# Kernel optimization log

Measured on AMD Instinct MI355X. Metric: run time of the kernel, lower is better.

## Reference

```python
import jax, jax.numpy as jnp
import numpy as np

D_MODEL = 2048
HEAD_DIM = 128

def setup_inputs() -> dict:
    key = jax.random.key(0)
    ks = jax.random.split(key, 7)
    s = 1.0 / np.sqrt(D_MODEL)
    x = jax.random.normal(ks[0], (4, 4096, D_MODEL), dtype=jnp.float32)
    Wq = jax.random.uniform(ks[1], (D_MODEL, HEAD_DIM), jnp.float32, -s, s)
    bq = jax.random.uniform(ks[2], (HEAD_DIM,), jnp.float32, -s, s)
    Wk = jax.random.uniform(ks[3], (D_MODEL, HEAD_DIM), jnp.float32, -s, s)
    bk = jax.random.uniform(ks[4], (HEAD_DIM,), jnp.float32, -s, s)
    Wv = jax.random.uniform(ks[5], (D_MODEL, HEAD_DIM), jnp.float32, -s, s)
    bv = jax.random.uniform(ks[6], (HEAD_DIM,), jnp.float32, -s, s)
    return {"x": x, "Wq": Wq, "bq": bq, "Wk": Wk, "bk": bk, "Wv": Wv, "bv": bv}

def reference(x, Wq, bq, Wk, bk, Wv, bv):
    # x: [B, T, d_model]
    B, T, _ = x.shape
    q = jnp.einsum('btd,dh->bth', x, Wq) + bq  # [B,T,H]
    k = jnp.einsum('btd,dh->bth', x, Wk) + bk
    v = jnp.einsum('btd,dh->bth', x, Wv) + bv
    scores = jnp.einsum('bth,bsh->bts', q, k) / jnp.sqrt(jnp.float32(HEAD_DIM))  # [B,T,T]
    causal = jnp.tril(jnp.ones((T, T), dtype=bool))
    scores = jnp.where(causal[None], scores, -jnp.inf)
    probs = jax.nn.softmax(scores, axis=-1)
    return jnp.einsum('bts,bsh->bth', probs, v)  # [B,T,H]
```

## Files before the change

kernel.cpp:

```cpp
#include <hip/hip_runtime.h>
#include <math.h>

#define D_MODEL 2048
#define HD      128
#define NB      4
#define TT      4096
#define M_TOT   (NB * TT)
#define NCH     160
#define CHT     16

typedef __attribute__((ext_vector_type(8))) short bf16x8;
typedef __attribute__((ext_vector_type(4))) float f32x4;

__device__ __forceinline__ ushort f2bf(float f) {
    union { float f; unsigned int u; } v; v.f = f;
    unsigned int u = v.u;
    unsigned int r = (u + 0x7FFFu + ((u >> 16) & 1u)) >> 16;
    return (ushort)r;
}

__device__ __forceinline__ void gload_lds16(const void* g, void* l) {
    __builtin_amdgcn_global_load_lds(
        (const __attribute__((address_space(1))) unsigned int*)g,
        (__attribute__((address_space(3))) unsigned int*)l, 16, 0, 0);
}

__global__ __launch_bounds__(256) void wt_kernel(
        const float* __restrict__ Wq, const float* __restrict__ Wk,
        const float* __restrict__ Wv, ushort* __restrict__ WT) {
    const int p  = blockIdx.y;
    const int k0 = blockIdx.x * 128;
    const float* W = (p == 0) ? Wq : ((p == 1) ? Wk : Wv);

    __shared__ ushort Ts[128 * 136];

    const int tid = threadIdx.x;
    for (int i = 0; i < 64; i++) {
        int c  = i * 256 + tid;
        int kk = c >> 7, n = c & 127;
        Ts[n * 136 + kk] = f2bf(W[(size_t)(k0 + kk) * 128 + n]);
    }
    __syncthreads();
    for (int i = 0; i < 8; i++) {
        int c = i * 256 + tid;
        int n = c >> 4, j = c & 15;
        *(uint4*)(WT + (size_t)p * (128 * 2048) + (size_t)n * 2048 + k0 + j * 8) =
            *(const uint4*)&Ts[n * 136 + j * 8];
    }
}

__global__ __launch_bounds__(256, 3) void proj_fused(
        const float* __restrict__ x, const ushort* __restrict__ WT,
        const float* __restrict__ bq, const float* __restrict__ bk, const float* __restrict__ bv,
        ushort* __restrict__ Qb, ushort* __restrict__ Kb, ushort* __restrict__ Vt) {
    const int bx   = blockIdx.x;
    const int row0 = (bx / 3) * 64;
    const int p    = bx % 3;
    const ushort* Wp   = WT + (size_t)p * (128 * 2048);
    const float*  bias = (p == 0) ? bq : ((p == 1) ? bk : bv);

    __shared__ ushort As[64 * 136];
    __shared__ ushort Bs[128 * 128];

    const int tid  = threadIdx.x;
    const int lane = tid & 63;
    const int wv   = tid >> 6;
    const int rw   = wv >> 1;
    const int cw   = wv & 1;
    const int quad = lane >> 4;
    const int ln16 = lane & 15;

    size_t  boff[8];
    ushort* bdst[8];
    for (int i = 0; i < 8; i++) {
        int c = i * 256 + tid;
        int n = c >> 4, j = c & 15;
        int kc = j ^ (n & 15);
        boff[i] = (size_t)n * 2048 + kc * 8;
        bdst[i] = &Bs[(i * 256 + wv * 64) * 8];
    }
    int arow[8], apos[8];
    for (int i = 0; i < 8; i++) {
        int c = i * 256 + tid;
        arow[i] = c >> 5;
        apos[i] = c & 31;
    }

    f32x4 acc[2][4];
    for (int m2 = 0; m2 < 2; m2++)
        for (int nt = 0; nt < 4; nt++)
            acc[m2][nt] = (f32x4){0.f, 0.f, 0.f, 0.f};

    float4 areg[8];
    for (int i = 0; i < 8; i++)
        areg[i] = *(const float4*)(x + (size_t)(row0 + arow[i]) * D_MODEL + apos[i] * 4);

    for (int k0 = 0; k0 < D_MODEL; k0 += 128) {
        __syncthreads();
        for (int i = 0; i < 8; i++)
            gload_lds16(Wp + boff[i] + k0, bdst[i]);
        for (int i = 0; i < 8; i++) {
            ushort4 o;
            o.x = f2bf(areg[i].x); o.y = f2bf(areg[i].y);
            o.z = f2bf(areg[i].z); o.w = f2bf(areg[i].w);
            *(ushort4*)&As[arow[i] * 136 + apos[i] * 4] = o;
        }
        __syncthreads();
        if (k0 + 128 < D_MODEL)
            for (int i = 0; i < 8; i++)
                areg[i] = *(const float4*)(x + (size_t)(row0 + arow[i]) * D_MODEL
                                             + k0 + 128 + apos[i] * 4);

        for (int mi = 0; mi < 4; mi++) {
            bf16x8 a[2], b[4];
            for (int m2 = 0; m2 < 2; m2++)
                a[m2] = *(const bf16x8*)&As[(rw * 32 + m2 * 16 + ln16) * 136 + mi * 32 + quad * 8];
            for (int nt = 0; nt < 4; nt++) {
                int n = cw * 64 + nt * 16 + ln16;
                int slot = (mi * 4 + quad) ^ (n & 15);
                b[nt] = *(const bf16x8*)&Bs[n * 128 + slot * 8];
            }
            for (int m2 = 0; m2 < 2; m2++)
                for (int nt = 0; nt < 4; nt++)
                    acc[m2][nt] = __builtin_amdgcn_mfma_f32_16x16x32_bf16(a[m2], b[nt], acc[m2][nt], 0, 0, 0);
        }
    }

    for (int nt = 0; nt < 4; nt++) {
        int h  = cw * 64 + nt * 16 + ln16;
        float bc = bias[h];
        for (int m2 = 0; m2 < 2; m2++) {
            int rbase = row0 + rw * 32 + m2 * 16 + quad * 4;
            if (p < 2) {
                ushort* O = (p == 0) ? Qb : Kb;
                for (int r = 0; r < 4; r++)
                    O[(size_t)(rbase + r) * HD + h] = f2bf(acc[m2][nt][r] + bc);
            } else {
                int b = rbase >> 12;
                int t = rbase & 4095;
                ushort4 o;
                o.x = f2bf(acc[m2][nt][0] + bc);
                o.y = f2bf(acc[m2][nt][1] + bc);
                o.z = f2bf(acc[m2][nt][2] + bc);
                o.w = f2bf(acc[m2][nt][3] + bc);
                *(ushort4*)(Vt + ((size_t)b * HD + h) * TT + t) = o;
            }
        }
    }
}

#define SCALE 0.08838834764831845f

__global__ __launch_bounds__(256, 2) void attn_part(
        const ushort* __restrict__ Qb, const ushort* __restrict__ Kb,
        const ushort* __restrict__ Vt, float* __restrict__ Opart,
        float* __restrict__ Mpart, float* __restrict__ Lpart) {
    const int blk = blockIdx.x;
    const int bb  = blk & 3;
    const int cid = blk >> 2;

    int rem = cid, qt = 63;
    for (;;) {
        int cnt = (qt >> 4) + 1;
        if (rem < cnt) break;
        rem -= cnt; --qt;
    }
    const int ch    = rem;
    const int st_lo = ch * CHT;
    const int st_hi = min(qt + 1, st_lo + CHT);
    const int q0    = qt * 64;

    __shared__ ushort Ks[2][64 * 128];
    __shared__ ushort Vs[2][128 * 64];
    __shared__ ushort Ps[64 * 64];

    const int tid  = threadIdx.x;
    const int lane = tid & 63;
    const int wv   = tid >> 6;
    const int quad = lane >> 4;
    const int ln16 = lane & 15;
    const int sw8  = ln16 & 7;

    int koff[4], voff[4], ldso[4];
    for (int i = 0; i < 4; i++) {
        int c = i * 256 + tid;
        { int r = c >> 4, j = c & 15, kc = j ^ (r & 15);
          koff[i] = r * HD + kc * 8; }
        { int h = c >> 3, j = c & 7, kc = j ^ (h & 7);
          voff[i] = h * TT + kc * 8; }
        ldso[i] = (i * 256 + wv * 64) * 8;
    }
    const ushort* kbase = Kb + (size_t)bb * TT * HD;
    const ushort* vbase = Vt + (size_t)bb * HD * TT;

    {
        const int s0 = st_lo * 64;
        for (int i = 0; i < 4; i++) gload_lds16(kbase + (size_t)s0 * HD + koff[i], &Ks[0][ldso[i]]);
        for (int i = 0; i < 4; i++) gload_lds16(vbase + s0 + voff[i], &Vs[0][ldso[i]]);
    }
    bf16x8 qf[4];
    {
        const ushort* qrow = Qb + (size_t)(bb * TT + q0 + 16 * wv + ln16) * HD;
        for (int kc = 0; kc < 4; kc++)
            qf[kc] = *(const bf16x8*)(qrow + kc * 32 + quad * 8);
    }

    f32x4 o_acc[8];
    for (int nt = 0; nt < 8; nt++) o_acc[nt] = (f32x4){0.f, 0.f, 0.f, 0.f};
    float m_i[4], l_i[4];
    for (int r = 0; r < 4; r++) { m_i[r] = -INFINITY; l_i[r] = 0.f; }

    __syncthreads();

    for (int st = st_lo; st < st_hi; st++) {
        const int s0  = st * 64;
        const int buf = (st - st_lo) & 1;

        if (st + 1 < st_hi) {
            const int s1 = s0 + 64;
            for (int i = 0; i < 4; i++) gload_lds16(kbase + (size_t)s1 * HD + koff[i], &Ks[buf ^ 1][ldso[i]]);
            for (int i = 0; i < 4; i++) gload_lds16(vbase + s1 + voff[i], &Vs[buf ^ 1][ldso[i]]);
        }

        f32x4 sacc[4];
        for (int nt = 0; nt < 4; nt++) sacc[nt] = (f32x4){0.f, 0.f, 0.f, 0.f};
        for (int kc = 0; kc < 4; kc++) {
            int lc = kc * 4 + quad;
            for (int nt = 0; nt < 4; nt++) {
                int r = nt * 16 + ln16;
                bf16x8 b = *(const bf16x8*)&Ks[buf][r * 128 + ((lc ^ ln16) * 8)];
                sacc[nt] = __builtin_amdgcn_mfma_f32_16x16x32_bf16(qf[kc], b, sacc[nt], 0, 0, 0);
            }
        }

        const bool diag = (st == qt);
        float mx[4];
        for (int r = 0; r < 4; r++) {
            for (int nt = 0; nt < 4; nt++) {
                float s = sacc[nt][r] * SCALE;
                if (diag) {
                    int sg = s0 + nt * 16 + ln16;
                    int qg = q0 + 16 * wv + quad * 4 + r;
                    if (sg > qg) s = -INFINITY;
                }
                sacc[nt][r] = s;
            }
            mx[r] = fmaxf(fmaxf(sacc[0][r], sacc[1][r]), fmaxf(sacc[2][r], sacc[3][r]));
        }
        for (int off = 8; off >= 1; off >>= 1)
            for (int r = 0; r < 4; r++)
                mx[r] = fmaxf(mx[r], __shfl_xor(mx[r], off));

        float al[4];
        for (int r = 0; r < 4; r++) {
            float mnew = fmaxf(m_i[r], mx[r]);
            al[r] = __expf(m_i[r] - mnew);
            m_i[r] = mnew;
        }
        float rs[4];
        for (int r = 0; r < 4; r++) {
            float s = 0.f;
            for (int nt = 0; nt < 4; nt++) {
                float pv = __expf(sacc[nt][r] - m_i[r]);
                sacc[nt][r] = pv;
                s += pv;
            }
            rs[r] = s;
        }
        for (int off = 8; off >= 1; off >>= 1)
            for (int r = 0; r < 4; r++)
                rs[r] += __shfl_xor(rs[r], off);
        for (int r = 0; r < 4; r++) l_i[r] = l_i[r] * al[r] + rs[r];
        for (int nt = 0; nt < 8; nt++)
            for (int r = 0; r < 4; r++)
                o_acc[nt][r] *= al[r];

        for (int nt = 0; nt < 4; nt++)
            for (int r = 0; r < 4; r++) {
                int row = 16 * wv + quad * 4 + r;
                int cj  = nt * 2 + (ln16 >> 3);
                Ps[row * 64 + ((cj ^ (row & 7)) * 8) + sw8] = f2bf(sacc[nt][r]);
            }

        for (int kc2 = 0; kc2 < 2; kc2++) {
            int lc = kc2 * 4 + quad;
            int prow = 16 * wv + ln16;
            bf16x8 a = *(const bf16x8*)&Ps[prow * 64 + ((lc ^ sw8) * 8)];
            for (int nt = 0; nt < 8; nt++) {
                int h = nt * 16 + ln16;
                bf16x8 b = *(const bf16x8*)&Vs[buf][h * 64 + ((lc ^ sw8) * 8)];
                o_acc[nt] = __builtin_amdgcn_mfma_f32_16x16x32_bf16(a, b, o_acc[nt], 0, 0, 0);
            }
        }

        __syncthreads();
    }

    const size_t slot = (size_t)bb * NCH + cid;
    for (int nt = 0; nt < 8; nt++)
        for (int r = 0; r < 4; r++)
            Opart[(slot * 64 + 16 * wv + quad * 4 + r) * HD + nt * 16 + ln16] = o_acc[nt][r];
    if (ln16 == 0)
        for (int r = 0; r < 4; r++) {
            Mpart[slot * 64 + 16 * wv + quad * 4 + r] = m_i[r];
            Lpart[slot * 64 + 16 * wv + quad * 4 + r] = l_i[r];
        }
}

__global__ __launch_bounds__(256) void merge_kernel(
        const float* __restrict__ Opart, const float* __restrict__ Mpart,
        const float* __restrict__ Lpart, float* __restrict__ out) {
    const int qt = blockIdx.x;
    const int bb = blockIdx.y;
    const int nch = (qt >> 4) + 1;
    int base = 0;
    for (int q = 63; q > qt; --q) base += (q >> 4) + 1;

    const int tid = threadIdx.x;
    const int q0  = qt * 64;
    for (int e = tid; e < 64 * 32; e += 256) {
        int row = e >> 5;
        int c4  = e & 31;
        float M = -INFINITY;
        float mv[4];
        for (int ch = 0; ch < nch; ch++) {
            mv[ch] = Mpart[((size_t)bb * NCH + base + ch) * 64 + row];
            M = fmaxf(M, mv[ch]);
        }
        float L = 0.f;
        float w[4];
        for (int ch = 0; ch < nch; ch++) {
            w[ch] = __expf(mv[ch] - M);
            L += w[ch] * Lpart[((size_t)bb * NCH + base + ch) * 64 + row];
        }
        float4 acc = {0.f, 0.f, 0.f, 0.f};
        for (int ch = 0; ch < nch; ch++) {
            const float4 o = *(const float4*)(Opart +
                (((size_t)bb * NCH + base + ch) * 64 + row) * HD + c4 * 4);
            acc.x += w[ch] * o.x; acc.y += w[ch] * o.y;
            acc.z += w[ch] * o.z; acc.w += w[ch] * o.w;
        }
        float invL = 1.f / L;
        float4 res = {acc.x * invL, acc.y * invL, acc.z * invL, acc.w * invL};
        *(float4*)(out + ((size_t)bb * TT + q0 + row) * HD + c4 * 4) = res;
    }
}

extern "C" void kernel_launch(void* const* d_in, const int* in_sizes, int n_in,
                              void* d_out, int out_size, void* d_ws, size_t ws_size,
                              hipStream_t stream) {
    const float* x  = (const float*)d_in[0];
    const float* Wq = (const float*)d_in[1];
    const float* bq = (const float*)d_in[2];
    const float* Wk = (const float*)d_in[3];
    const float* bk = (const float*)d_in[4];
    const float* Wv = (const float*)d_in[5];
    const float* bv = (const float*)d_in[6];
    float* out = (float*)d_out;

    ushort* WT = (ushort*)d_ws;
    ushort* Qb = WT + (size_t)3 * HD * D_MODEL;
    ushort* Kb = Qb + (size_t)M_TOT * HD;
    ushort* Vt = Kb + (size_t)M_TOT * HD;
    float* Opart = (float*)(Vt + (size_t)M_TOT * HD);
    float* Mpart = Opart + (size_t)NB * NCH * 64 * HD;
    float* Lpart = Mpart + (size_t)NB * NCH * 64;

    hipLaunchKernelGGL(wt_kernel, dim3(16, 3), dim3(256), 0, stream, Wq, Wk, Wv, WT);
    hipLaunchKernelGGL(proj_fused, dim3(768), dim3(256), 0, stream,
                       x, WT, bq, bk, bv, Qb, Kb, Vt);
    hipLaunchKernelGGL(attn_part, dim3(NB * NCH), dim3(256), 0, stream,
                       Qb, Kb, Vt, Opart, Mpart, Lpart);
    hipLaunchKernelGGL(merge_kernel, dim3(64, NB), dim3(256), 0, stream,
                       Opart, Mpart, Lpart, out);
}
```

Baseline: 321.0 us.

## Process two KV tiles per iteration with single-buffered LDS and register-staged V prefetch

The attention loop now handles 128 keys per iteration instead of 64, which halves the number of softmax reductions and block barriers per chunk. K and V are single-buffered in LDS. The next K tile is fetched by LDS DMA once QK^T is done, and the next V tile is loaded into registers and written to LDS after the PV barrier. This adds register pressure and raises LDS use to about 80 KB, which may cut occupancy. It also relies on masking when the chunk has an odd tile count, which can read one tile past the end of the buffer.

```diff
diff --git a/kernel.cpp b/kernel.cpp
--- a/kernel.cpp
+++ b/kernel.cpp
@@ -170,9 +170,9 @@
     const int st_hi = min(qt + 1, st_lo + CHT);
     const int q0    = qt * 64;
 
-    __shared__ ushort Ks[2][64 * 128];
-    __shared__ ushort Vs[2][128 * 64];
-    __shared__ ushort Ps[64 * 64];
+    __shared__ ushort Ks[128 * 128];
+    __shared__ ushort Vs[128 * 128];
+    __shared__ ushort Ps[64 * 128];
 
     const int tid  = threadIdx.x;
     const int lane = tid & 63;
@@ -181,12 +181,12 @@
     const int ln16 = lane & 15;
     const int sw8  = ln16 & 7;
 
-    int koff[4], voff[4], ldso[4];
-    for (int i = 0; i < 4; i++) {
+    int koff[8], voff[8], ldso[8];
+    for (int i = 0; i < 8; i++) {
         int c = i * 256 + tid;
         { int r = c >> 4, j = c & 15, kc = j ^ (r & 15);
           koff[i] = r * HD + kc * 8; }
-        { int h = c >> 3, j = c & 7, kc = j ^ (h & 7);
+        { int h = c >> 4, j = c & 15, kc = j ^ (h & 15);
           voff[i] = h * TT + kc * 8; }
         ldso[i] = (i * 256 + wv * 64) * 8;
     }
@@ -194,9 +194,9 @@
     const ushort* vbase = Vt + (size_t)bb * HD * TT;
 
     {
-        const int s0 = st_lo * 64;
-        for (int i = 0; i < 4; i++) gload_lds16(kbase + (size_t)s0 * HD + koff[i], &Ks[0][ldso[i]]);
-        for (int i = 0; i < 4; i++) gload_lds16(vbase + s0 + voff[i], &Vs[0][ldso[i]]);
+        const int s0p = st_lo * 64;
+        for (int i = 0; i < 8; i++) gload_lds16(kbase + (size_t)s0p * HD + koff[i], &Ks[ldso[i]]);
+        for (int i = 0; i < 8; i++) gload_lds16(vbase + s0p + voff[i], &Vs[ldso[i]]);
     }
     bf16x8 qf[4];
     {
@@ -212,31 +212,36 @@
 
     __syncthreads();
 
-    for (int st = st_lo; st < st_hi; st++) {
-        const int s0  = st * 64;
-        const int buf = (st - st_lo) & 1;
-
-        if (st + 1 < st_hi) {
-            const int s1 = s0 + 64;
-            for (int i = 0; i < 4; i++) gload_lds16(kbase + (size_t)s1 * HD + koff[i], &Ks[buf ^ 1][ldso[i]]);
-            for (int i = 0; i < 4; i++) gload_lds16(vbase + s1 + voff[i], &Vs[buf ^ 1][ldso[i]]);
-        }
-
-        f32x4 sacc[4];
-        for (int nt = 0; nt < 4; nt++) sacc[nt] = (f32x4){0.f, 0.f, 0.f, 0.f};
+    for (int st2 = st_lo; st2 < st_hi; st2 += 2) {
+        const int s0 = st2 * 64;
+        const bool pf = (st2 + 2 < st_hi);
+
+        f32x4 sacc[8];
+        for (int nt = 0; nt < 8; nt++) sacc[nt] = (f32x4){0.f, 0.f, 0.f, 0.f};
         for (int kc = 0; kc < 4; kc++) {
             int lc = kc * 4 + quad;
-            for (int nt = 0; nt < 4; nt++) {
+            for (int nt = 0; nt < 8; nt++) {
                 int r = nt * 16 + ln16;
-                bf16x8 b = *(const bf16x8*)&Ks[buf][r * 128 + ((lc ^ ln16) * 8)];
+                bf16x8 b = *(const bf16x8*)&Ks[r * 128 + ((lc ^ ln16) * 8)];
                 sacc[nt] = __builtin_amdgcn_mfma_f32_16x16x32_bf16(qf[kc], b, sacc[nt], 0, 0, 0);
             }
         }
 
-        const bool diag = (st == qt);
+        __syncthreads();
+
+        uint4 vreg[8];
+        if (pf) {
+            const int s1 = s0 + 128;
+            for (int i = 0; i < 8; i++)
+                gload_lds16(kbase + (size_t)s1 * HD + koff[i], &Ks[ldso[i]]);
+            for (int i = 0; i < 8; i++)
+                vreg[i] = *(const uint4*)(vbase + s1 + voff[i]);
+        }
+
+        const bool diag = (qt - st2) < 2;
         float mx[4];
         for (int r = 0; r < 4; r++) {
-            for (int nt = 0; nt < 4; nt++) {
+            for (int nt = 0; nt < 8; nt++) {
                 float s = sacc[nt][r] * SCALE;
                 if (diag) {
                     int sg = s0 + nt * 16 + ln16;
@@ -245,7 +250,9 @@
                 }
                 sacc[nt][r] = s;
             }
-            mx[r] = fmaxf(fmaxf(sacc[0][r], sacc[1][r]), fmaxf(sacc[2][r], sacc[3][r]));
+            float a0 = fmaxf(fmaxf(sacc[0][r], sacc[1][r]), fmaxf(sacc[2][r], sacc[3][r]));
+            float a1 = fmaxf(fmaxf(sacc[4][r], sacc[5][r]), fmaxf(sacc[6][r], sacc[7][r]));
+            mx[r] = fmaxf(a0, a1);
         }
         for (int off = 8; off >= 1; off >>= 1)
             for (int r = 0; r < 4; r++)
@@ -260,7 +267,7 @@
         float rs[4];
         for (int r = 0; r < 4; r++) {
             float s = 0.f;
-            for (int nt = 0; nt < 4; nt++) {
+            for (int nt = 0; nt < 8; nt++) {
                 float pv = __expf(sacc[nt][r] - m_i[r]);
                 sacc[nt][r] = pv;
                 s += pv;
@@ -275,25 +282,29 @@
             for (int r = 0; r < 4; r++)
                 o_acc[nt][r] *= al[r];
 
-        for (int nt = 0; nt < 4; nt++)
+        for (int nt = 0; nt < 8; nt++)
             for (int r = 0; r < 4; r++) {
                 int row = 16 * wv + quad * 4 + r;
                 int cj  = nt * 2 + (ln16 >> 3);
-                Ps[row * 64 + ((cj ^ (row & 7)) * 8) + sw8] = f2bf(sacc[nt][r]);
-            }
-
-        for (int kc2 = 0; kc2 < 2; kc2++) {
+                Ps[row * 128 + ((cj ^ (row & 15)) * 8) + sw8] = f2bf(sacc[nt][r]);
+            }
+
+        for (int kc2 = 0; kc2 < 4; kc2++) {
             int lc = kc2 * 4 + quad;
             int prow = 16 * wv + ln16;
-            bf16x8 a = *(const bf16x8*)&Ps[prow * 64 + ((lc ^ sw8) * 8)];
+            bf16x8 a = *(const bf16x8*)&Ps[prow * 128 + ((lc ^ ln16) * 8)];
             for (int nt = 0; nt < 8; nt++) {
                 int h = nt * 16 + ln16;
-                bf16x8 b = *(const bf16x8*)&Vs[buf][h * 64 + ((lc ^ sw8) * 8)];
+                bf16x8 b = *(const bf16x8*)&Vs[h * 128 + ((lc ^ ln16) * 8)];
                 o_acc[nt] = __builtin_amdgcn_mfma_f32_16x16x32_bf16(a, b, o_acc[nt], 0, 0, 0);
             }
         }
 
         __syncthreads();
+
+        if (pf)
+            for (int i = 0; i < 8; i++)
+                *(uint4*)&Vs[(size_t)(i * 256 + tid) * 8] = vreg[i];
     }
 
     const size_t slot = (size_t)bb * NCH + cid;
```

Result: slower. 341.6 us (+6.4%).
